# Kernel optimization log

Hardware: AMD Instinct MI355X
Metric: run time of the kernel (lower is better)

## Reference

```python
import jax, jax.numpy as jnp
import numpy as np

B, C, D, H, W = 2, 512, 32, 32, 32
L, CTX = 256, 768
NH, HD, G = 8, 64, 8
EPS = 1e-5


def group_norm(x, w, b):
    Bb, Cc, Dd, Hh, Ww = x.shape
    xg = x.reshape(Bb, G, Cc // G, Dd, Hh, Ww)
    mu = xg.mean(axis=(2, 3, 4, 5), keepdims=True)
    var = xg.var(axis=(2, 3, 4, 5), keepdims=True)
    xn = ((xg - mu) * jax.lax.rsqrt(var + EPS)).reshape(Bb, Cc, Dd, Hh, Ww)
    return xn * w[None, :, None, None, None] + b[None, :, None, None, None]


def layer_norm(x, w, b):
    mu = x.mean(axis=-1, keepdims=True)
    var = x.var(axis=-1, keepdims=True)
    return (x - mu) * jax.lax.rsqrt(var + EPS) * w + b


def setup_inputs() -> dict:
    key = jax.random.key(0)
    ks = jax.random.split(key, 8)
    s = 0.02  # weight init scale
    return {
        "x": jax.random.normal(ks[0], (B, C, D, H, W), jnp.float32),
        "context": jax.random.normal(ks[1], (B, L, CTX), jnp.float32),
        "gn_w": jnp.ones((C,), jnp.float32),
        "gn_b": jnp.zeros((C,), jnp.float32),
        "ln_w": jnp.ones((CTX,), jnp.float32),
        "ln_b": jnp.zeros((CTX,), jnp.float32),
        "q_w": jax.random.normal(ks[2], (C, C), jnp.float32) * s,
        "q_b": jnp.zeros((C,), jnp.float32),
        "k_w": jax.random.normal(ks[3], (C, CTX), jnp.float32) * s,
        "k_b": jnp.zeros((C,), jnp.float32),
        "v_w": jax.random.normal(ks[4], (C, CTX), jnp.float32) * s,
        "v_b": jnp.zeros((C,), jnp.float32),
        "proj_w": jax.random.normal(ks[5], (C, C), jnp.float32) * s,
        "proj_b": jnp.zeros((C,), jnp.float32),
    }


def reference(x, context, gn_w, gn_b, ln_w, ln_b, q_w, q_b, k_w, k_b, v_w, v_b, proj_w, proj_b):
    Bb, Cc, Dd, Hh, Ww = x.shape
    S = Dd * Hh * Ww
    h = group_norm(x, gn_w, gn_b)
    ctx = layer_norm(context, ln_w, ln_b)
    # 1x1 Conv3d == per-voxel linear over channels
    q = jnp.einsum('oc,bcdhw->bodhw', q_w, h) + q_b[None, :, None, None, None]
    q = q.reshape(Bb, NH, HD, S)                                        # (b,h,e,s)
    k = (ctx @ k_w.T + k_b).reshape(Bb, L, NH, HD).transpose(0, 2, 1, 3)  # (b,h,l,e)
    v = (ctx @ v_w.T + v_b).reshape(Bb, L, NH, HD).transpose(0, 2, 1, 3)  # (b,h,l,e)
    scale = HD ** -0.5
    attn = jnp.einsum('bhes,bhle->bhsl', q, k) * scale                  # (b,h,S,L)
    attn = jax.nn.softmax(attn, axis=-1)
    out = jnp.einsum('bhsl,bhle->bhes', attn, v).reshape(Bb, Cc, Dd, Hh, Ww)
    out = jnp.einsum('oc,bcdhw->bodhw', proj_w, out) + proj_b[None, :, None, None, None]
    return out + x
```

## Files before the change

kernel.cpp:

```cpp
#include <hip/hip_runtime.h>

typedef unsigned short u16;
typedef unsigned int u32;
typedef __attribute__((ext_vector_type(4))) float f32x4;
typedef __attribute__((ext_vector_type(8))) short bf16x8;
typedef __attribute__((ext_vector_type(8))) u16 u16x8;
typedef __attribute__((ext_vector_type(4))) u16 u16x4;
typedef __attribute__((ext_vector_type(4))) u32 u32x4;

#define DEVI __device__ __forceinline__

constexpr int C_ = 512, S_ = 32768, L_ = 256, CTX_ = 768;

DEVI u16 f2b(float f) {
    union { float f; unsigned u; } x; x.f = f;
    unsigned r = x.u + 0x7fffu + ((x.u >> 16) & 1u);
    return (u16)(r >> 16);
}

DEVI f32x4 mfma16(bf16x8 a, bf16x8 b, f32x4 c) {
    return __builtin_amdgcn_mfma_f32_16x16x32_bf16(a, b, c, 0, 0, 0);
}

DEVI void gload16(const void* g, void* l) {
    __builtin_amdgcn_global_load_lds(
        (const __attribute__((address_space(1))) void*)g,
        (__attribute__((address_space(3))) void*)l, 16, 0, 0);
}

DEVI u32 cvtpk(float lo, float hi) {
    u32 d;
    asm("v_cvt_pk_bf16_f32 %0, %1, %2" : "=v"(d) : "v"(lo), "v"(hi));
    return d;
}
DEVI void pl32(u32& a, u32& b) {
    asm volatile("v_permlane32_swap_b32 %0, %1" : "+v"(a), "+v"(b));
}
DEVI void pl16(u32& a, u32& b) {
    asm volatile("v_permlane16_swap_b32 %0, %1" : "+v"(a), "+v"(b));
}

__global__ __launch_bounds__(256) void prep_small(
    const float* __restrict__ a0, const float* __restrict__ a1,
    const float* __restrict__ a2, const float* __restrict__ a3,
    u16* __restrict__ o0, u16* __restrict__ o1,
    u16* __restrict__ o2, u16* __restrict__ o3,
    const float* __restrict__ ctx, const float* __restrict__ lw,
    const float* __restrict__ lb, u16* __restrict__ cn)
{
    const int which = blockIdx.y, tid = threadIdx.x;
    if (which < 4) {
        const float* src = which == 0 ? a0 : which == 1 ? a1 : which == 2 ? a2 : a3;
        u16* dst = which == 0 ? o0 : which == 1 ? o1 : which == 2 ? o2 : o3;
        int n4 = (which == 1 || which == 2) ? (512 * 768 / 4) : (512 * 512 / 4);
        int i = blockIdx.x * 256 + tid;
        if (i < n4) {
            float4 v = ((const float4*)src)[i];
            u16x4 o; o[0] = f2b(v.x); o[1] = f2b(v.y); o[2] = f2b(v.z); o[3] = f2b(v.w);
            ((u16x4*)dst)[i] = o;
        }
        return;
    }
    const int row = blockIdx.x;
    const float* p = ctx + (size_t)row * CTX_;
    float v0 = p[tid], v1 = p[tid + 256], v2 = p[tid + 512];
    float s1 = v0 + v1 + v2, s2 = v0 * v0 + v1 * v1 + v2 * v2;
    for (int m = 1; m < 64; m <<= 1) { s1 += __shfl_xor(s1, m); s2 += __shfl_xor(s2, m); }
    __shared__ float a1s[4], a2s[4];
    int w = tid >> 6, lane = tid & 63;
    if (lane == 0) { a1s[w] = s1; a2s[w] = s2; }
    __syncthreads();
    s1 = a1s[0] + a1s[1] + a1s[2] + a1s[3];
    s2 = a2s[0] + a2s[1] + a2s[2] + a2s[3];
    const float invN = 1.0f / 768.0f;
    float mu = s1 * invN, rstd = rsqrtf(s2 * invN - mu * mu + 1e-5f);
    u16* o = cn + (size_t)row * CTX_;
    o[tid]       = f2b((v0 - mu) * rstd * lw[tid]       + lb[tid]);
    o[tid + 256] = f2b((v1 - mu) * rstd * lw[tid + 256] + lb[tid + 256]);
    o[tid + 512] = f2b((v2 - mu) * rstd * lw[tid + 512] + lb[tid + 512]);
}

__global__ __launch_bounds__(256) void gn_partial(const float* __restrict__ x,
                                                  float* __restrict__ part)
{
    const int bg = blockIdx.y, blk = blockIdx.x, tid = threadIdx.x;
    const float* base = x + (size_t)bg * 64 * S_ + (size_t)blk * 1024 + tid * 4;
    float s1 = 0.f, s2 = 0.f;
    for (int c = 0; c < 64; ++c) {
        float4 v = *(const float4*)(base + (size_t)c * S_);
        s1 += v.x + v.y + v.z + v.w;
        s2 += v.x * v.x + v.y * v.y + v.z * v.z + v.w * v.w;
    }
    for (int m = 1; m < 64; m <<= 1) { s1 += __shfl_xor(s1, m); s2 += __shfl_xor(s2, m); }
    __shared__ float a1[4], a2[4];
    int w = tid >> 6, lane = tid & 63;
    if (lane == 0) { a1[w] = s1; a2[w] = s2; }
    __syncthreads();
    if (tid == 0) {
        part[(bg * 32 + blk) * 2 + 0] = a1[0] + a1[1] + a1[2] + a1[3];
        part[(bg * 32 + blk) * 2 + 1] = a2[0] + a2[1] + a2[2] + a2[3];
    }
}

__global__ __launch_bounds__(64) void gn_final_coef(
    const float* __restrict__ part, const float* __restrict__ gw,
    const float* __restrict__ gb, float* __restrict__ ca, float* __restrict__ cb)
{
    int bg = blockIdx.x, tid = threadIdx.x;
    float s1 = tid < 32 ? part[(bg * 32 + tid) * 2] : 0.f;
    float s2 = tid < 32 ? part[(bg * 32 + tid) * 2 + 1] : 0.f;
    for (int m = 1; m < 32; m <<= 1) { s1 += __shfl_xor(s1, m); s2 += __shfl_xor(s2, m); }
    const float invN = 1.0f / (64.0f * (float)S_);
    float mu = __shfl(s1, 0) * invN;
    float var = __shfl(s2, 0) * invN - mu * mu;
    float rs = rsqrtf(var + 1e-5f);
    int z = bg >> 3, c = (bg & 7) * 64 + tid;
    float a = rs * gw[c];
    ca[z * 512 + c] = a;
    cb[z * 512 + c] = gb[c] - mu * a;
}

template <int MODE, bool SWAP>
__global__ __launch_bounds__(256, 4) void gemm_nt(
    const u16* __restrict__ A, const u16* __restrict__ Bp,
    const float* __restrict__ bias, void* __restrict__ outp,
    const float* __restrict__ resid, int K, int ldo,
    size_t aStride, size_t bStride, size_t oStride, float scale,
    const u16* __restrict__ Bp2, const float* __restrict__ bias2,
    void* __restrict__ outp2)
{
    __shared__ __align__(16) u16 lA[2][4096];
    __shared__ __align__(16) u16 lB[2][4096];
    const int tid = threadIdx.x;
    const int w = tid >> 6, lane = tid & 63;
    const int g = lane >> 4, r = lane & 15;

    const int nx = gridDim.x, nxy = nx * gridDim.y;
    const int raw = blockIdx.x + nx * blockIdx.y;
    const int tile = (raw & 7) * (nxy >> 3) + (raw >> 3);
    const int bx = tile % nx, by = tile / nx;
    const int m0 = (SWAP ? by : bx) * 128, n0 = (SWAP ? bx : by) * 128;
    const int z = blockIdx.z;
    A += (size_t)z * aStride;
    const u16* Bsel = Bp;
    if constexpr (MODE == 3) { if (z) Bsel = Bp2; }
    Bsel += (size_t)z * bStride;

    const int l8 = lane & 7, lh = lane >> 3;
    const int u_ = l8 ^ lh;
    const int mro = (lh << 1) + (u_ >> 2);
    const int kco = (u_ & 3) * 8;
    const int wr = w >> 1, wc = w & 1;
    const int nt = K >> 5;

    f32x4 acc[4][4];
#pragma unroll
    for (int m = 0; m < 4; ++m)
#pragma unroll
        for (int n = 0; n < 4; ++n) acc[m][n] = f32x4{0.f, 0.f, 0.f, 0.f};

#define STAGE_B(t, bi_) {                                                      \
    size_t ko_ = (size_t)((t) * 32 + kco);                                     \
    _Pragma("unroll")                                                          \
    for (int j = 0; j < 2; ++j) {                                              \
        int grow_ = w * 32 + j * 16 + mro;                                     \
        gload16(Bsel + (size_t)(n0 + grow_) * K + ko_,                         \
                &lB[bi_][(w * 16 + j * 8) << 6]);                              \
    } }

#define STAGE_A(t, bi_) {                                                      \
    size_t ko_ = (size_t)((t) * 32 + kco);                                     \
    _Pragma("unroll")                                                          \
    for (int j = 0; j < 2; ++j) {                                              \
        int grow_ = w * 32 + j * 16 + mro;                                     \
        gload16(A + (size_t)(m0 + grow_) * K + ko_,                            \
                &lA[bi_][(w * 16 + j * 8) << 6]);                              \
    } }

    const float* xA = nullptr;
    const float* cAp = nullptr;
    const float* cBp = nullptr;
    int cp2 = 0, sb = 0, zc = 0;
    f32x4 a00{}, a01{}, a10{}, a11{};
    float2 ka{}, kb{};
    if constexpr (MODE == 4) {
        xA = resid + (size_t)z * ((size_t)C_ * S_);
        cAp = bias2;
        cBp = (const float*)outp2;
        cp2 = (tid >> 4) * 2;
        sb = (tid & 15) * 8;
        zc = z * 512;
    }

#define LOAD_A4(t) {                                                           \
    int c0n_ = (t) * 32 + cp2;                                                 \
    const float* r0_ = xA + (size_t)c0n_ * S_ + m0 + sb;                       \
    a00 = *(const f32x4*)r0_;  a01 = *(const f32x4*)(r0_ + 4);                 \
    a10 = *(const f32x4*)(r0_ + S_); a11 = *(const f32x4*)(r0_ + S_ + 4);      \
    ka = *(const float2*)&cAp[zc + c0n_];                                      \
    kb = *(const float2*)&cBp[zc + c0n_]; }

#define WRITE_A4(bi_) {                                                        \
    _Pragma("unroll")                                                          \
    for (int j = 0; j < 8; ++j) {                                              \
        float v0_ = ((j < 4) ? a00[j] : a01[j - 4]) * ka.x + kb.x;             \
        float v1_ = ((j < 4) ? a10[j] : a11[j - 4]) * ka.y + kb.y;             \
        int mm_ = sb + j;                                                      \
        int idx_ = ((mm_ >> 1) << 6)                                           \
            + (((((mm_ & 1) << 2) + (cp2 >> 3)) ^ ((mm_ >> 1) & 7)) << 3)      \
            + (cp2 & 7);                                                       \
        *(u32*)&lA[bi_][idx_] = cvtpk(v0_, v1_);                               \
    } }

    if constexpr (MODE == 4) {
        STAGE_B(0, 0);
        LOAD_A4(0);
        WRITE_A4(0);
    } else {
        STAGE_A(0, 0);
        STAGE_B(0, 0);
    }
    __syncthreads();

    for (int t = 0; t < nt; ++t) {
        const int cur = t & 1;
        if (t + 1 < nt) {
            STAGE_B(t + 1, cur ^ 1);
            if constexpr (MODE == 4) { LOAD_A4(t + 1); }
            else                     { STAGE_A(t + 1, cur ^ 1); }
        }
        bf16x8 af[4], bf_[4];
#pragma unroll
        for (int m = 0; m < 4; ++m) {
            int row = wr * 32 + m * 8 + (r >> 1);
            int slot = (((r & 1) << 2) + g) ^ ((r >> 1) & 7);
            af[m] = *(const bf16x8*)&lA[cur][(row << 6) + (slot << 3)];
        }
#pragma unroll
        for (int n = 0; n < 4; ++n) {
            int row = wc * 32 + n * 8 + (r >> 1);
            int slot = (((r & 1) << 2) + g) ^ ((r >> 1) & 7);
            bf_[n] = *(const bf16x8*)&lB[cur][(row << 6) + (slot << 3)];
        }
#pragma unroll
        for (int m = 0; m < 4; ++m)
#pragma unroll
            for (int n = 0; n < 4; ++n)
                acc[m][n] = mfma16(bf_[n], af[m], acc[m][n]);
        if constexpr (MODE == 4) { if (t + 1 < nt) WRITE_A4(cur ^ 1); }
        __syncthreads();
    }
#undef STAGE_A
#undef STAGE_B
#undef LOAD_A4
#undef WRITE_A4

    if constexpr (MODE == 0 || MODE == 4) {
        u16* ob = (u16*)outp + (size_t)z * oStride;
#pragma unroll
        for (int m = 0; m < 4; ++m) {
            int gm = m0 + wr * 64 + m * 16 + r;
#pragma unroll
            for (int n = 0; n < 4; ++n) {
                int gn0 = n0 + wc * 64 + n * 16 + g * 4;
                float4 bn = *(const float4*)&bias[gn0];
                u32 w0 = cvtpk(acc[m][n][0] * scale + bn.x * scale,
                               acc[m][n][1] * scale + bn.y * scale);
                u32 w1 = cvtpk(acc[m][n][2] * scale + bn.z * scale,
                               acc[m][n][3] * scale + bn.w * scale);
                *(uint2*)&ob[(size_t)gm * ldo + gn0] = make_uint2(w0, w1);
            }
        }
    } else if constexpr (MODE == 2) {
        float* of = (float*)outp + (size_t)z * oStride;
        const float* rs = resid + (size_t)z * oStride;
#pragma unroll
        for (int m = 0; m < 4; ++m) {
            int gm = m0 + wr * 64 + m * 16 + r;
            float bm = bias[gm];
#pragma unroll
            for (int n = 0; n < 4; ++n) {
                int gn0 = n0 + wc * 64 + n * 16 + g * 4;
                size_t idx = (size_t)gm * ldo + gn0;
                float4 rv = *(const float4*)&rs[idx];
                float4 o4;
                o4.x = acc[m][n][0] + bm + rv.x;
                o4.y = acc[m][n][1] + bm + rv.y;
                o4.z = acc[m][n][2] + bm + rv.z;
                o4.w = acc[m][n][3] + bm + rv.w;
                *(float4*)&of[idx] = o4;
            }
        }
    } else if constexpr (MODE == 3) {
        if (z == 0) {
            u16* ob = (u16*)outp;
#pragma unroll
            for (int m = 0; m < 4; ++m) {
                int gm = m0 + wr * 64 + m * 16 + r;
#pragma unroll
                for (int n = 0; n < 4; ++n) {
                    int gn0 = n0 + wc * 64 + n * 16 + g * 4;
                    float4 bn = *(const float4*)&bias[gn0];
                    u32 w0 = cvtpk(acc[m][n][0] + bn.x, acc[m][n][1] + bn.y);
                    u32 w1 = cvtpk(acc[m][n][2] + bn.z, acc[m][n][3] + bn.w);
                    *(uint2*)&ob[(size_t)gm * ldo + gn0] = make_uint2(w0, w1);
                }
            }
        } else {
            u16* ob = (u16*)outp2;
#pragma unroll
            for (int m = 0; m < 4; ++m) {
                int gm = m0 + wr * 64 + m * 16 + r;
                int bb = gm >> 8, l = gm & 255;
#pragma unroll
                for (int n = 0; n < 4; ++n) {
                    int gn0 = n0 + wc * 64 + n * 16 + g * 4;
#pragma unroll
                    for (int i = 0; i < 4; ++i)
                        ob[((size_t)(bb * 512 + gn0 + i)) * 256 + l] =
                            f2b(acc[m][n][i] + bias2[gn0 + i]);
                }
            }
        }
    }
}

__global__ __launch_bounds__(512, 2) void attn_kernel(
    const u16* __restrict__ q, const u16* __restrict__ kk,
    const u16* __restrict__ vv, u16* __restrict__ ao)
{
    __shared__ __align__(16) u16 sm[32768];
    const int tid = threadIdx.x;
    const int w = tid >> 6, lane = tid & 63;
    const int g = lane >> 4, r = lane & 15;
    const int bh = blockIdx.y, b = bh >> 3, h = bh & 7;
    const int s0 = blockIdx.x * 256;

    {
        const u16* kbase = kk + ((size_t)b * L_) * C_ + h * 64;
#pragma unroll
        for (int j = 0; j < 4; ++j) {
            int idx = j * 512 + tid;
            int l = idx >> 3, ch = idx & 7;
            u16x8 val = *(const u16x8*)(kbase + (size_t)l * C_ + ch * 8);
            *(u16x8*)&sm[l * 64 + ((ch ^ (l & 7)) << 3)] = val;
        }
        const u16* vbase = vv + ((size_t)bh * 64) * 256;
#pragma unroll
        for (int j = 0; j < 4; ++j) {
            int idx = j * 512 + tid;
            int e = idx >> 5, ch = idx & 31;
            u16x8 val = *(const u16x8*)(vbase + (size_t)e * 256 + ch * 8);
            *(u16x8*)&sm[16384 + e * 256 + ((ch ^ (e & 7)) << 3)] = val;
        }
    }

    const int sw = s0 + w * 32;
    bf16x8 qf[2][2];
#pragma unroll
    for (int m = 0; m < 2; ++m)
#pragma unroll
        for (int kt = 0; kt < 2; ++kt)
            qf[m][kt] = *(const bf16x8*)(q + ((size_t)(b * S_ + sw + m * 16 + r)) * C_
                                         + h * 64 + kt * 32 + g * 8);
    __syncthreads();

    f32x4 accs[2][16];
#pragma unroll
    for (int m = 0; m < 2; ++m)
#pragma unroll
        for (int n = 0; n < 16; ++n) accs[m][n] = f32x4{0.f, 0.f, 0.f, 0.f};
    __builtin_amdgcn_s_setprio(1);
#pragma unroll
    for (int n = 0; n < 16; ++n) {
#pragma unroll
        for (int kt = 0; kt < 2; ++kt) {
            int c = kt * 4 + g;
            bf16x8 kf = *(const bf16x8*)&sm[(n * 16 + r) * 64 + ((c ^ (r & 7)) << 3)];
#pragma unroll
            for (int m = 0; m < 2; ++m) accs[m][n] = mfma16(kf, qf[m][kt], accs[m][n]);
        }
    }
    __builtin_amdgcn_s_setprio(0);

    float inv[2];
#pragma unroll
    for (int m = 0; m < 2; ++m) {
        float mx = accs[m][0][0];
#pragma unroll
        for (int n = 0; n < 16; ++n)
#pragma unroll
            for (int i = 0; i < 4; ++i) mx = fmaxf(mx, accs[m][n][i]);
        mx = fmaxf(mx, __shfl_xor(mx, 16));
        mx = fmaxf(mx, __shfl_xor(mx, 32));
        float sum = 0.f;
#pragma unroll
        for (int n = 0; n < 16; ++n)
#pragma unroll
            for (int i = 0; i < 4; ++i) {
                float e = __expf(accs[m][n][i] - mx);
                accs[m][n][i] = e; sum += e;
            }
        sum += __shfl_xor(sum, 16);
        sum += __shfl_xor(sum, 32);
        inv[m] = 1.0f / sum;
    }

    f32x4 acco[2][4];
#pragma unroll
    for (int m = 0; m < 2; ++m)
#pragma unroll
        for (int n = 0; n < 4; ++n) acco[m][n] = f32x4{0.f, 0.f, 0.f, 0.f};

#pragma unroll
    for (int c = 0; c < 8; ++c) {
        bf16x8 pa[2];
#pragma unroll
        for (int m = 0; m < 2; ++m) {
            u32 x0 = cvtpk(accs[m][2 * c][0] * inv[m], accs[m][2 * c][1] * inv[m]);
            u32 x1 = cvtpk(accs[m][2 * c][2] * inv[m], accs[m][2 * c][3] * inv[m]);
            u32 y0 = cvtpk(accs[m][2 * c + 1][0] * inv[m], accs[m][2 * c + 1][1] * inv[m]);
            u32 y1 = cvtpk(accs[m][2 * c + 1][2] * inv[m], accs[m][2 * c + 1][3] * inv[m]);
            pl32(x0, y0);
            pl32(x1, y1);
            pl16(x0, y0);
            pl16(x1, y1);
            u32x4 pw; pw[0] = x0; pw[1] = x1; pw[2] = y0; pw[3] = y1;
            pa[m] = *(bf16x8*)&pw;
        }
        bf16x8 vf[4];
#pragma unroll
        for (int n = 0; n < 4; ++n) {
            int e = n * 16 + r;
            vf[n] = *(const bf16x8*)&sm[16384 + e * 256 + (((c * 4 + g) ^ (r & 7)) << 3)];
        }
        __builtin_amdgcn_s_setprio(1);
#pragma unroll
        for (int m = 0; m < 2; ++m)
#pragma unroll
            for (int n = 0; n < 4; ++n)
                acco[m][n] = mfma16(vf[n], pa[m], acco[m][n]);
        __builtin_amdgcn_s_setprio(0);
    }

#pragma unroll
    for (int m = 0; m < 2; ++m) {
        const size_t rowb = ((size_t)(b * S_ + sw + m * 16 + r)) * C_ + h * 64;
#pragma unroll
        for (int n = 0; n < 4; ++n) {
            u32 w0 = cvtpk(acco[m][n][0], acco[m][n][1]);
            u32 w1 = cvtpk(acco[m][n][2], acco[m][n][3]);
            *(uint2*)&ao[rowb + n * 16 + g * 4] = make_uint2(w0, w1);
        }
    }
}

extern "C" void kernel_launch(void* const* d_in, const int* in_sizes, int n_in,
                              void* d_out, int out_size, void* d_ws, size_t ws_size,
                              hipStream_t stream)
{
    (void)in_sizes; (void)n_in; (void)out_size; (void)ws_size;
    const float* x    = (const float*)d_in[0];
    const float* ctx  = (const float*)d_in[1];
    const float* gn_w = (const float*)d_in[2];
    const float* gn_b = (const float*)d_in[3];
    const float* ln_w = (const float*)d_in[4];
    const float* ln_b = (const float*)d_in[5];
    const float* q_w  = (const float*)d_in[6];
    const float* q_b  = (const float*)d_in[7];
    const float* k_w  = (const float*)d_in[8];
    const float* k_b  = (const float*)d_in[9];
    const float* v_w  = (const float*)d_in[10];
    const float* v_b  = (const float*)d_in[11];
    const float* p_w  = (const float*)d_in[12];
    const float* p_b  = (const float*)d_in[13];
    float* out = (float*)d_out;

    char* ws = (char*)d_ws;
    constexpr size_t WS_WQ   = 0;
    constexpr size_t WS_WK   = WS_WQ + (size_t)512 * 512 * 2;
    constexpr size_t WS_WV   = WS_WK + (size_t)512 * 768 * 2;
    constexpr size_t WS_WP   = WS_WV + (size_t)512 * 768 * 2;
    constexpr size_t WS_PART = WS_WP + (size_t)512 * 512 * 2;
    constexpr size_t WS_CA   = WS_PART + (size_t)16 * 64 * 2 * 4;
    constexpr size_t WS_CB   = WS_CA + 4096;
    constexpr size_t WS_CTXN = WS_CB + 4096;
    constexpr size_t WS_K    = WS_CTXN + (size_t)512 * 768 * 2;
    constexpr size_t WS_V    = WS_K + (size_t)2 * 8 * 256 * 64 * 2;
    constexpr size_t WS_Q    = WS_V + (size_t)2 * 8 * 256 * 64 * 2;
    constexpr size_t WS_H    = WS_Q + (size_t)2 * 32768 * 512 * 2;

    u16* wq = (u16*)(ws + WS_WQ);
    u16* wk = (u16*)(ws + WS_WK);
    u16* wv = (u16*)(ws + WS_WV);
    u16* wp = (u16*)(ws + WS_WP);
    float* part  = (float*)(ws + WS_PART);
    float* coefA = (float*)(ws + WS_CA);
    float* coefB = (float*)(ws + WS_CB);
    u16* ctxn = (u16*)(ws + WS_CTXN);
    u16* kt   = (u16*)(ws + WS_K);
    u16* vt   = (u16*)(ws + WS_V);
    u16* qt   = (u16*)(ws + WS_Q);
    u16* ao   = (u16*)(ws + WS_H);

    const size_t bsc = (size_t)S_ * C_;

    gn_partial<<<dim3(32, 16), 256, 0, stream>>>(x, part);
    prep_small<<<dim3(512, 5), 256, 0, stream>>>(q_w, k_w, v_w, p_w,
                                                 wq, wk, wv, wp,
                                                 ctx, ln_w, ln_b, ctxn);
    gn_final_coef<<<16, 64, 0, stream>>>(part, gn_w, gn_b, coefA, coefB);
    gemm_nt<4, true><<<dim3(4, 256, 2), 256, 0, stream>>>(
        nullptr, wq, q_b, qt, x, 512, 512, 0, 0, bsc, 0.125f,
        nullptr, coefA, coefB);
    gemm_nt<3, false><<<dim3(4, 4, 2), 256, 0, stream>>>(
        ctxn, wk, k_b, kt, nullptr, 768, 512, 0, 0, 0, 1.0f,
        wv, v_b, vt);
    attn_kernel<<<dim3(128, 16), 512, 0, stream>>>(qt, kt, vt, ao);
    gemm_nt<2, false><<<dim3(4, 256, 2), 256, 0, stream>>>(
        wp, ao, p_b, out, x, 512, S_, 0, bsc, bsc, 1.0f,
        nullptr, nullptr, nullptr);
}
```

Measured before the change: 282.7 us.

## Replace projection GEMM with 256x256-tile 8-wave double-buffered kernel

The output projection GEMM moves from the generic 128-tile gemm_nt path to a dedicated kernel with 512 threads and 256x256 output tiles. It double-buffers LDS with an XOR-swizzled layout, issues next-tile global loads between MFMA quarters, and remaps block indices for L2 locality. Bias and residual are fused into a float4 epilogue. The larger tiles should cut redundant A/B traffic per FLOP, at the cost of heavy register use (occupancy 1) and fewer blocks.

```diff
diff --git a/kernel.cpp b/kernel.cpp
--- a/kernel.cpp
+++ b/kernel.cpp
@@ -321,6 +321,122 @@
                             f2b(acc[m][n][i] + bias2[gn0 + i]);
                 }
             }
+        }
+    }
+}
+
+__global__ __launch_bounds__(512, 1) void gemm8_proj(
+    const u16* __restrict__ Aw, const u16* __restrict__ Bm,
+    const float* __restrict__ bias, float* __restrict__ outp,
+    const float* __restrict__ resid)
+{
+    __shared__ __align__(16) u16 LA[2][2][2][4096];
+    __shared__ __align__(16) u16 LB[2][2][2][4096];
+    const int tid = threadIdx.x;
+    const int w = tid >> 6, lane = tid & 63;
+    const int g = lane >> 4, r = lane & 15;
+
+    const int raw = blockIdx.x + 2 * blockIdx.y;
+    const int tile = (raw & 7) * 32 + (raw >> 3);
+    const int m0 = (tile & 1) * 256, n0 = (tile >> 1) * 256;
+    const int z = blockIdx.z;
+    const size_t bsc = (size_t)S_ * C_;
+    const u16* Bz = Bm + (size_t)z * bsc;
+
+    const int l8 = lane & 7, lh = lane >> 3;
+    const int u_ = l8 ^ lh;
+    const int mro = (lh << 1) + (u_ >> 2);
+    const int kco = (u_ & 3) * 8;
+    const int grow = w * 16 + mro;
+    const int wr = w >> 2, wc = w & 3;
+
+    f32x4 acc[8][4];
+#pragma unroll
+    for (int mi = 0; mi < 8; ++mi)
+#pragma unroll
+        for (int ni = 0; ni < 4; ++ni) acc[mi][ni] = f32x4{0.f, 0.f, 0.f, 0.f};
+
+#define STGA(bi, half, panel, kt)                                              \
+    gload16(Aw + (size_t)(m0 + (half) * 128 + grow) * 512                      \
+                + (kt) * 64 + (panel) * 32 + kco,                              \
+            &LA[bi][half][panel][w << 9]);
+#define STGB(bi, half, panel, kt)                                              \
+    gload16(Bz + (size_t)(n0 + (half) * 128 + grow) * 512                      \
+                + (kt) * 64 + (panel) * 32 + kco,                              \
+            &LB[bi][half][panel][w << 9]);
+
+    STGA(0, 0, 0, 0); STGA(0, 0, 1, 0); STGA(0, 1, 0, 0); STGA(0, 1, 1, 0);
+    STGB(0, 0, 0, 0); STGB(0, 0, 1, 0); STGB(0, 1, 0, 0); STGB(0, 1, 1, 0);
+    asm volatile("s_waitcnt vmcnt(0)" ::: "memory");
+    __builtin_amdgcn_s_barrier();
+
+    const int fro = r >> 1;
+    const int sl = (((r & 1) << 2) + g) ^ ((r >> 1) & 7);
+
+    for (int kt = 0; kt < 8; ++kt) {
+        const int buf = kt & 1, nb = buf ^ 1;
+        const bool more = (kt + 1 < 8);
+#pragma unroll
+        for (int q = 0; q < 4; ++q) {
+            const int mh = q >> 1, nh = q & 1;
+            bf16x8 af[4][2], bf[2][2];
+#pragma unroll
+            for (int i = 0; i < 4; ++i)
+#pragma unroll
+                for (int kk = 0; kk < 2; ++kk)
+                    af[i][kk] = *(const bf16x8*)
+                        &LA[buf][wr][kk][(((mh * 4 + i) * 8 + fro) << 6) + (sl << 3)];
+#pragma unroll
+            for (int j = 0; j < 2; ++j)
+#pragma unroll
+                for (int kk = 0; kk < 2; ++kk)
+                    bf[j][kk] = *(const bf16x8*)
+                        &LB[buf][wc >> 1][kk]
+                           [((((wc & 1) * 4 + nh * 2 + j) * 8 + fro) << 6) + (sl << 3)];
+            if (more) {
+                if (q == 0) {
+                    STGA(nb, 0, 0, kt + 1); STGA(nb, 0, 1, kt + 1);
+                    STGA(nb, 1, 0, kt + 1); STGA(nb, 1, 1, kt + 1);
+                } else if (q == 1) {
+                    STGB(nb, 0, 0, kt + 1); STGB(nb, 0, 1, kt + 1);
+                    STGB(nb, 1, 0, kt + 1); STGB(nb, 1, 1, kt + 1);
+                }
+            }
+            __builtin_amdgcn_s_barrier();
+            __builtin_amdgcn_s_setprio(1);
+#pragma unroll
+            for (int i = 0; i < 4; ++i)
+#pragma unroll
+                for (int j = 0; j < 2; ++j)
+#pragma unroll
+                    for (int kk = 0; kk < 2; ++kk)
+                        acc[mh * 4 + i][nh * 2 + j] =
+                            mfma16(bf[j][kk], af[i][kk], acc[mh * 4 + i][nh * 2 + j]);
+            __builtin_amdgcn_s_setprio(0);
+            if (q == 3 && more) asm volatile("s_waitcnt vmcnt(0)" ::: "memory");
+            __builtin_amdgcn_s_barrier();
+        }
+    }
+#undef STGA
+#undef STGB
+
+    float* of = outp + (size_t)z * bsc;
+    const float* rs = resid + (size_t)z * bsc;
+#pragma unroll
+    for (int mi = 0; mi < 8; ++mi) {
+        int gm = m0 + wr * 128 + mi * 16 + r;
+        float bm = bias[gm];
+#pragma unroll
+        for (int ni = 0; ni < 4; ++ni) {
+            int gn0 = n0 + wc * 64 + ni * 16 + g * 4;
+            size_t idx = (size_t)gm * S_ + gn0;
+            float4 rv = *(const float4*)&rs[idx];
+            float4 o4;
+            o4.x = acc[mi][ni][0] + bm + rv.x;
+            o4.y = acc[mi][ni][1] + bm + rv.y;
+            o4.z = acc[mi][ni][2] + bm + rv.z;
+            o4.w = acc[mi][ni][3] + bm + rv.w;
+            *(float4*)&of[idx] = o4;
         }
     }
 }
@@ -517,7 +633,5 @@
         ctxn, wk, k_b, kt, nullptr, 768, 512, 0, 0, 0, 1.0f,
         wv, v_b, vt);
     attn_kernel<<<dim3(128, 16), 512, 0, stream>>>(qt, kt, vt, ao);
-    gemm_nt<2, false><<<dim3(4, 256, 2), 256, 0, stream>>>(
-        wp, ao, p_b, out, x, 512, S_, 0, bsc, bsc, 1.0f,
-        nullptr, nullptr, nullptr);
-}
+    gemm8_proj<<<dim3(2, 128, 2), 512, 0, stream>>>(wp, ao, p_b, out, x);
+}
```

Result: no change. 287.0 us (+1.5%).
